# Optimization experiments

Measured on AMD Instinct MI355X. Metric: run time of the kernel, lower is better.

Reference implementation:

```python
import jax, jax.numpy as jnp
import numpy as np

SEQ, BATCH, D_MODEL, HEADS = 2048, 4, 1024, 16
D_K = D_MODEL // HEADS
SCALE = 1.0 / np.sqrt(D_K).astype(np.float32)


def setup_inputs() -> dict:
    key = jax.random.key(0)
    ks = jax.random.split(key, 12)
    s = 0.02
    inp = {
        "query": jax.random.normal(ks[0], (SEQ, BATCH, D_MODEL), jnp.float32),
        "key": jax.random.normal(ks[1], (SEQ, BATCH, D_MODEL), jnp.float32),
        "value": jax.random.normal(ks[2], (SEQ, BATCH, D_MODEL), jnp.float32),
        # causal mask [seq_q, seq_k, 1]; batch dim broadcasts per prepare_mask
        "mask": jnp.tril(jnp.ones((SEQ, SEQ), jnp.int32))[:, :, None],
        "Wq": jax.random.normal(ks[3], (D_MODEL, D_MODEL), jnp.float32) * s,
        "bq": jnp.zeros((D_MODEL,), jnp.float32),
        "Wk": jax.random.normal(ks[4], (D_MODEL, D_MODEL), jnp.float32) * s,
        "bk": jnp.zeros((D_MODEL,), jnp.float32),
        "Wv": jax.random.normal(ks[5], (D_MODEL, D_MODEL), jnp.float32) * s,
        "bv": jnp.zeros((D_MODEL,), jnp.float32),
        "Wo": jax.random.normal(ks[6], (D_MODEL, D_MODEL), jnp.float32) * s,
        "bo": jnp.zeros((D_MODEL,), jnp.float32),
    }
    return inp


def _heads(x, W, b):
    # [s, b, d_model] -> [s, b, h, d_k]
    y = jnp.einsum('sbd,de->sbe', x, W.T) + b
    return y.reshape(x.shape[0], x.shape[1], HEADS, D_K)


def reference(query, key, value, mask, Wq, bq, Wk, bk, Wv, bv, Wo, bo):
    seq_len, batch_size, _ = query.shape
    q = _heads(query, Wq, bq)
    k = _heads(key, Wk, bk)
    v = _heads(value, Wv, bv)
    # scores [i, j, b, h]
    scores = jnp.einsum('ibhd,jbhd->ijbh', q, k) * SCALE
    m = mask[:, :, :, None]  # [sq, sk, b_or_1, 1]
    scores = jnp.where(m == 0, jnp.float32(-jnp.inf), scores)
    attn = jax.nn.softmax(scores, axis=1)  # softmax over key dim j
    x = jnp.einsum('ijbh,jbhd->ibhd', attn, v)
    x = x.reshape(seq_len, batch_size, D_MODEL)
    return jnp.einsum('sbd,de->sbe', x, Wo.T) + bo
```

## Files before the change

### kernel.cpp

```cpp
#include <hip/hip_runtime.h>
#include <hip/hip_bf16.h>

#define SEQ 2048
#define BATCH 4
#define DM 1024
#define HEADS 16
#define DK 64
#define NBH 64
#define SC_LOG2E (0.125f * 1.4426950408889634f)

typedef unsigned short u16;
typedef __attribute__((ext_vector_type(8))) short bf16x8;
typedef __attribute__((ext_vector_type(4))) float f32x4;

__device__ inline u16 f2bf(float f) {
    unsigned int u = __builtin_bit_cast(unsigned int, f);
    u += 0x7fffu + ((u >> 16) & 1u);
    return (u16)(u >> 16);
}
__device__ inline float fexp2(float x) {
    float r; asm("v_exp_f32 %0, %1" : "=v"(r) : "v"(x)); return r;
}
__device__ inline unsigned pkbf(float a, float b) {
    unsigned r; asm("v_cvt_pk_bf16_f32 %0, %1, %2" : "=v"(r) : "v"(a), "v"(b)); return r;
}

__global__ __launch_bounds__(256)
void conv_bf16(const float* __restrict__ q, const float* __restrict__ k,
               const float* __restrict__ v, const float* __restrict__ wq,
               const float* __restrict__ wk, const float* __restrict__ wv,
               const float* __restrict__ wo,
               u16* __restrict__ oq, u16* __restrict__ ok, u16* __restrict__ ov,
               u16* __restrict__ ow)
{
    const size_t A8 = (size_t)SEQ * BATCH * DM / 8;
    const size_t W8 = (size_t)DM * DM / 8;
    const size_t total = 3 * A8 + 4 * W8;
    for (size_t i = (size_t)blockIdx.x * 256 + threadIdx.x; i < total;
         i += (size_t)gridDim.x * 256) {
        const float* src; u16* dst; size_t off;
        if (i < A8)          { src = q; dst = oq; off = i; }
        else if (i < 2 * A8) { src = k; dst = ok; off = i - A8; }
        else if (i < 3 * A8) { src = v; dst = ov; off = i - 2 * A8; }
        else {
            size_t j = i - 3 * A8;
            int wsel = (int)(j >> 17);
            off = j & (W8 - 1);
            src = wsel == 0 ? wq : wsel == 1 ? wk : wsel == 2 ? wv : wo;
            dst = ow + (size_t)wsel * DM * DM;
        }
        float4 a = ((const float4*)src)[off * 2];
        float4 b = ((const float4*)src)[off * 2 + 1];
        uint4 w;
        w.x = pkbf(a.x, a.y); w.y = pkbf(a.z, a.w);
        w.z = pkbf(b.x, b.y); w.w = pkbf(b.z, b.w);
        *(uint4*)(dst + off * 8) = w;
    }
}

__device__ inline void gstage(const u16* __restrict__ src, u16* dst,
                              int wave, int lane) {
    #pragma unroll
    for (int i = 0; i < 4; ++i) {
        int ci = (i * 4 + wave) * 64 + lane;
        int row = ci >> 3, ch = ci & 7;
        const u16* g = src + (size_t)row * 1024 + ((ch ^ (row & 7)) << 3);
        u16* l = dst + (i * 4 + wave) * 512;
        __builtin_amdgcn_global_load_lds(
            (const __attribute__((address_space(1))) unsigned int*)g,
            (__attribute__((address_space(3))) unsigned int*)l, 16, 0, 0);
    }
}
__device__ inline bf16x8 rdt(const u16* t, int row, int ch) {
    return *(const bf16x8*)(t + row * 64 + ((ch ^ (row & 7)) << 3));
}

template<int MODE>
__global__ __launch_bounds__(256, 2)
void gemm_bf(const u16* __restrict__ A, const u16* __restrict__ B,
             const float* __restrict__ bias, void* __restrict__ Out, float oscale)
{
    __shared__ __align__(16) u16 sA[2][128 * 64];
    __shared__ __align__(16) u16 sB[2][128 * 64];
    const int tid  = threadIdx.x;
    const int lane = tid & 63, wave = tid >> 6;
    const int wr = (wave >> 1) * 64, wc = (wave & 1) * 64;
    const int l15 = lane & 15, lg = lane >> 4;
    const int row0 = blockIdx.x * 128, col0 = blockIdx.y * 128;
    const u16* Abase = A + (size_t)row0 * 1024;
    const u16* Bbase = B + (size_t)col0 * 1024;

    f32x4 acc[4][4];
    #pragma unroll
    for (int m = 0; m < 4; ++m)
        #pragma unroll
        for (int n = 0; n < 4; ++n) acc[m][n] = (f32x4){0.f, 0.f, 0.f, 0.f};

    gstage(Abase, sA[0], wave, lane);
    gstage(Bbase, sB[0], wave, lane);
    __syncthreads();

    int cur = 0;
    for (int kt = 0; kt < 16; ++kt) {
        if (kt < 15) {
            gstage(Abase + (kt + 1) * 64, sA[cur ^ 1], wave, lane);
            gstage(Bbase + (kt + 1) * 64, sB[cur ^ 1], wave, lane);
        }
        #pragma unroll
        for (int s = 0; s < 2; ++s) {
            bf16x8 af[4], bf[4];
            #pragma unroll
            for (int m = 0; m < 4; ++m)
                af[m] = rdt(sA[cur], wr + m * 16 + l15, s * 4 + lg);
            #pragma unroll
            for (int n = 0; n < 4; ++n)
                bf[n] = rdt(sB[cur], wc + n * 16 + l15, s * 4 + lg);
            __builtin_amdgcn_s_setprio(1);
            #pragma unroll
            for (int m = 0; m < 4; ++m)
                #pragma unroll
                for (int n = 0; n < 4; ++n)
                    acc[m][n] = __builtin_amdgcn_mfma_f32_16x16x32_bf16(
                        af[m], bf[n], acc[m][n], 0, 0, 0);
            __builtin_amdgcn_s_setprio(0);
        }
        __syncthreads();
        cur ^= 1;
    }

    #pragma unroll
    for (int m = 0; m < 4; ++m) {
        #pragma unroll
        for (int n = 0; n < 4; ++n) {
            #pragma unroll
            for (int r = 0; r < 4; ++r) {
                int R = row0 + wr + m * 16 + lg * 4 + r;
                int E = col0 + wc + n * 16 + l15;
                float v = (acc[m][n][r] + bias[E]) * oscale;
                if (MODE == 2) {
                    ((float*)Out)[(size_t)R * 1024 + E] = v;
                } else {
                    int s = R >> 2, b = R & 3, hh = E >> 6, d = E & 63;
                    size_t idx = (MODE == 0)
                        ? ((size_t)(b * HEADS + hh) * SEQ + s) * DK + d
                        : ((size_t)(b * HEADS + hh) * DK + d) * SEQ + s;
                    ((u16*)Out)[idx] = f2bf(v);
                }
            }
        }
    }
}

__device__ inline void stage_tile(const u16* __restrict__ srcRow0, int srcStride,
                                  u16* tile, int wave, int lane) {
    #pragma unroll
    for (int i = 0; i < 2; ++i) {
        int row = wave * 16 + i * 8 + (lane >> 3);
        int chunk = (lane & 7) ^ (row & 7);
        const u16* g = srcRow0 + (size_t)row * srcStride + chunk * 8;
        u16* l = tile + (wave * 16 + i * 8) * 64;
        __builtin_amdgcn_global_load_lds(
            (const __attribute__((address_space(1))) unsigned int*)g,
            (__attribute__((address_space(3))) unsigned int*)l, 16, 0, 0);
    }
}
__device__ inline bf16x8 tread(const u16* tile, int row, int chunk) {
    return *(const bf16x8*)((const char*)tile + row * 128 + ((chunk ^ (row & 7)) << 4));
}

__global__ __launch_bounds__(256, 4)
void attn_fwd(const u16* __restrict__ Q, const u16* __restrict__ K,
              const u16* __restrict__ V, u16* __restrict__ X)
{
    __shared__ __align__(16) u16 sK[2][4096];
    __shared__ __align__(16) u16 sV[2][4096];
    __shared__ __align__(16) u16 plds[4][16 * 64];

    const int lin = blockIdx.x + 16 * blockIdx.y;
    const int xcd = lin & 7, ii = lin >> 3;
    const int bh  = (ii & 7) | (xcd << 3);
    const int tA  = ii >> 3;
    const int tB  = 31 - tA;
    const int b = bh >> 4, h = bh & 15;
    const int lane = threadIdx.x & 63, wave = threadIdx.x >> 6;
    const int l15 = lane & 15, lg = lane >> 4;
    const int qloc = wave * 16 + l15;
    const int swz  = (l15 & 7) << 4;
    const u16* Qh = Q + (size_t)bh * SEQ * DK;
    const u16* Kh = K + (size_t)bh * SEQ * DK;
    const u16* Vh = V + (size_t)bh * SEQ * DK;

    const int qA = tA * 64 + wave * 16, qB = tB * 64 + wave * 16;
    const bf16x8 qfA0 = *(const bf16x8*)&Qh[(size_t)(qA + l15) * DK + lg * 8];
    const bf16x8 qfA1 = *(const bf16x8*)&Qh[(size_t)(qA + l15) * DK + 32 + lg * 8];
    const bf16x8 qfB0 = *(const bf16x8*)&Qh[(size_t)(qB + l15) * DK + lg * 8];
    const bf16x8 qfB1 = *(const bf16x8*)&Qh[(size_t)(qB + l15) * DK + 32 + lg * 8];

    f32x4 oA[4], oB[4];
    #pragma unroll
    for (int n = 0; n < 4; ++n) {
        oA[n] = (f32x4){0.f, 0.f, 0.f, 0.f};
        oB[n] = (f32x4){0.f, 0.f, 0.f, 0.f};
    }
    float lsA = 0.f, lsB = 0.f;

    u16* pw = &plds[wave][0];

    auto compute = [&](const u16* kt, const u16* vt,
                       const bf16x8& q0v, const bf16x8& q1v,
                       f32x4* o, float& ls, bool diag) {
        f32x4 sc[4];
        #pragma unroll
        for (int c = 0; c < 4; ++c) sc[c] = (f32x4){0.f, 0.f, 0.f, 0.f};

        __builtin_amdgcn_s_setprio(1);
        #pragma unroll
        for (int c = 0; c < 4; ++c) {
            bf16x8 k0 = tread(kt, 16 * c + l15, lg);
            bf16x8 k1 = tread(kt, 16 * c + l15, 4 + lg);
            sc[c] = __builtin_amdgcn_mfma_f32_16x16x32_bf16(k0, q0v, sc[c], 0, 0, 0);
            sc[c] = __builtin_amdgcn_mfma_f32_16x16x32_bf16(k1, q1v, sc[c], 0, 0, 0);
        }
        __builtin_amdgcn_s_setprio(0);

        #pragma unroll
        for (int c = 0; c < 4; ++c) {
            float p[4];
            #pragma unroll
            for (int r = 0; r < 4; ++r) {
                float e = fexp2(sc[c][r]);
                if (diag) {
                    int kl = 16 * c + 4 * lg + r;
                    e = (kl <= qloc) ? e : 0.f;
                }
                p[r] = e;
                ls += e;
            }
            uint2 w;
            w.x = pkbf(p[0], p[1]);
            w.y = pkbf(p[2], p[3]);
            *(uint2*)((char*)pw + l15 * 128 + ((32 * c + 8 * lg) ^ swz)) = w;
        }
        asm volatile("s_waitcnt lgkmcnt(0)" ::: "memory");
        __builtin_amdgcn_sched_barrier(0);
        bf16x8 pf0 = *(const bf16x8*)((const char*)pw + l15 * 128 + ((16 * lg) ^ swz));
        bf16x8 pf1 = *(const bf16x8*)((const char*)pw + l15 * 128 + ((64 + 16 * lg) ^ swz));

        __builtin_amdgcn_s_setprio(1);
        #pragma unroll
        for (int n = 0; n < 4; ++n) {
            bf16x8 v0 = tread(vt, 16 * n + l15, lg);
            bf16x8 v1 = tread(vt, 16 * n + l15, 4 + lg);
            o[n] = __builtin_amdgcn_mfma_f32_16x16x32_bf16(pf0, v0, o[n], 0, 0, 0);
            o[n] = __builtin_amdgcn_mfma_f32_16x16x32_bf16(pf1, v1, o[n], 0, 0, 0);
        }
        __builtin_amdgcn_s_setprio(0);
    };

    stage_tile(Kh, DK, sK[0], wave, lane);
    stage_tile(Vh, SEQ, sV[0], wave, lane);
    __syncthreads();

    const int nst = tB + 1;
    int cur = 0;
    for (int blk = 0; blk < nst; ++blk) {
        if (blk + 1 < nst) {
            const int j1 = (blk + 1) * 64;
            stage_tile(Kh + (size_t)j1 * DK, DK, sK[cur ^ 1], wave, lane);
            stage_tile(Vh + j1, SEQ, sV[cur ^ 1], wave, lane);
        }
        if (blk <= tA)
            compute(sK[cur], sV[cur], qfA0, qfA1, oA, lsA, blk == tA);
        compute(sK[cur], sV[cur], qfB0, qfB1, oB, lsB, blk == tB);
        __syncthreads();
        cur ^= 1;
    }

    auto finish = [&](f32x4* o, float ls, int q0) {
        float tot = ls;
        tot += __shfl_xor(tot, 16, 64);
        tot += __shfl_xor(tot, 32, 64);
        float inv[4];
        #pragma unroll
        for (int r = 0; r < 4; ++r)
            inv[r] = 1.0f / __shfl(tot, lg * 4 + r, 64);
        #pragma unroll
        for (int n = 0; n < 4; ++n)
            #pragma unroll
            for (int r = 0; r < 4; ++r) {
                const int i = q0 + lg * 4 + r;
                X[((size_t)i * BATCH + b) * DM + h * DK + 16 * n + l15] =
                    f2bf(o[n][r] * inv[r]);
            }
    };
    finish(oA, lsA, qA);
    finish(oB, lsB, qB);
}

extern "C" void kernel_launch(void* const* d_in, const int* in_sizes, int n_in,
                              void* d_out, int out_size, void* d_ws, size_t ws_size,
                              hipStream_t stream) {
    const float* query = (const float*)d_in[0];
    const float* key   = (const float*)d_in[1];
    const float* value = (const float*)d_in[2];
    const float* Wq = (const float*)d_in[4];
    const float* bq = (const float*)d_in[5];
    const float* Wk = (const float*)d_in[6];
    const float* bk = (const float*)d_in[7];
    const float* Wv = (const float*)d_in[8];
    const float* bv = (const float*)d_in[9];
    const float* Wo = (const float*)d_in[10];
    const float* bo = (const float*)d_in[11];

    const size_t NELEM = (size_t)SEQ * BATCH * DM;
    const size_t WM    = (size_t)DM * DM;
    u16* S0  = (u16*)d_ws;
    u16* S1  = S0 + NELEM;
    u16* S2  = S1 + NELEM;
    u16* S3  = S2 + NELEM;
    u16* Wbf = S3 + NELEM;

    dim3 gg(64, 8), gb(256);
    hipLaunchKernelGGL(conv_bf16, dim3(2048), gb, 0, stream,
                       query, key, value, Wq, Wk, Wv, Wo, S0, S1, S2, Wbf);
    hipLaunchKernelGGL((gemm_bf<0>), gg, gb, 0, stream, S0, Wbf,          bq, S3, SC_LOG2E);
    hipLaunchKernelGGL((gemm_bf<0>), gg, gb, 0, stream, S1, Wbf + WM,     bk, S0, 1.0f);
    hipLaunchKernelGGL((gemm_bf<1>), gg, gb, 0, stream, S2, Wbf + 2 * WM, bv, S1, 1.0f);
    hipLaunchKernelGGL(attn_fwd, dim3(16, NBH), gb, 0, stream, S3, S0, S1, S2);
    hipLaunchKernelGGL((gemm_bf<2>), gg, gb, 0, stream, S2, Wbf + 3 * WM, bo, (float*)d_out, 1.0f);
}
```

Before: 176.7 us.

## Pair adjacent query tiles per block and interleave their MFMAs on shared K/V

Each block now takes two adjacent 64-row query tiles (t16*128 and +64) instead of the mirrored pair tA and 31-tA. One loop over key tiles runs QK^T and PV for both query tiles on each staged K/V tile, so both reuse the same LDS reads and their independent MFMAs can interleave. The explicit lgkmcnt wait and sched barrier before reading P are dropped, giving the scheduler more freedom. In exchange, work per block is no longer balanced (2 to 32 iterations); blocks are launched heaviest first to soften the tail.

Measured after the change: 184.1 us. 1.04x slower.

```diff
diff --git a/kernel.cpp b/kernel.cpp
--- a/kernel.cpp
+++ b/kernel.cpp
@@ -177,20 +177,20 @@
     __shared__ __align__(16) u16 plds[4][16 * 64];
 
     const int lin = blockIdx.x + 16 * blockIdx.y;
-    const int xcd = lin & 7, ii = lin >> 3;
-    const int bh  = (ii & 7) | (xcd << 3);
-    const int tA  = ii >> 3;
-    const int tB  = 31 - tA;
+    const int xcd = lin & 7;
+    const int bh  = xcd * 8 + ((lin >> 3) & 7);
+    const int t16 = 15 - (lin >> 6);
     const int b = bh >> 4, h = bh & 15;
     const int lane = threadIdx.x & 63, wave = threadIdx.x >> 6;
     const int l15 = lane & 15, lg = lane >> 4;
     const int qloc = wave * 16 + l15;
-    const int swz  = (l15 & 7) << 4;
+    const int swz = (l15 & 7) << 4;
     const u16* Qh = Q + (size_t)bh * SEQ * DK;
     const u16* Kh = K + (size_t)bh * SEQ * DK;
     const u16* Vh = V + (size_t)bh * SEQ * DK;
 
-    const int qA = tA * 64 + wave * 16, qB = tB * 64 + wave * 16;
+    const int qA = t16 * 128 + wave * 16;
+    const int qB = qA + 64;
     const bf16x8 qfA0 = *(const bf16x8*)&Qh[(size_t)(qA + l15) * DK + lg * 8];
     const bf16x8 qfA1 = *(const bf16x8*)&Qh[(size_t)(qA + l15) * DK + 32 + lg * 8];
     const bf16x8 qfB0 = *(const bf16x8*)&Qh[(size_t)(qB + l15) * DK + lg * 8];
@@ -203,26 +203,9 @@
         oB[n] = (f32x4){0.f, 0.f, 0.f, 0.f};
     }
     float lsA = 0.f, lsB = 0.f;
-
     u16* pw = &plds[wave][0];
 
-    auto compute = [&](const u16* kt, const u16* vt,
-                       const bf16x8& q0v, const bf16x8& q1v,
-                       f32x4* o, float& ls, bool diag) {
-        f32x4 sc[4];
-        #pragma unroll
-        for (int c = 0; c < 4; ++c) sc[c] = (f32x4){0.f, 0.f, 0.f, 0.f};
-
-        __builtin_amdgcn_s_setprio(1);
-        #pragma unroll
-        for (int c = 0; c < 4; ++c) {
-            bf16x8 k0 = tread(kt, 16 * c + l15, lg);
-            bf16x8 k1 = tread(kt, 16 * c + l15, 4 + lg);
-            sc[c] = __builtin_amdgcn_mfma_f32_16x16x32_bf16(k0, q0v, sc[c], 0, 0, 0);
-            sc[c] = __builtin_amdgcn_mfma_f32_16x16x32_bf16(k1, q1v, sc[c], 0, 0, 0);
-        }
-        __builtin_amdgcn_s_setprio(0);
-
+    auto expack = [&](f32x4* sc, bool diag, float& ls, bf16x8& pf0, bf16x8& pf1) {
         #pragma unroll
         for (int c = 0; c < 4; ++c) {
             float p[4];
@@ -241,37 +224,63 @@
             w.y = pkbf(p[2], p[3]);
             *(uint2*)((char*)pw + l15 * 128 + ((32 * c + 8 * lg) ^ swz)) = w;
         }
-        asm volatile("s_waitcnt lgkmcnt(0)" ::: "memory");
-        __builtin_amdgcn_sched_barrier(0);
-        bf16x8 pf0 = *(const bf16x8*)((const char*)pw + l15 * 128 + ((16 * lg) ^ swz));
-        bf16x8 pf1 = *(const bf16x8*)((const char*)pw + l15 * 128 + ((64 + 16 * lg) ^ swz));
+        pf0 = *(const bf16x8*)((const char*)pw + l15 * 128 + ((16 * lg) ^ swz));
+        pf1 = *(const bf16x8*)((const char*)pw + l15 * 128 + ((64 + 16 * lg) ^ swz));
+    };
+
+    const int NB = 2 * t16 + 2;
+    stage_tile(Kh, DK, sK[0], wave, lane);
+    stage_tile(Vh, SEQ, sV[0], wave, lane);
+    __syncthreads();
+
+    int cur = 0;
+    for (int j = 0; j < NB; ++j) {
+        if (j + 1 < NB) {
+            stage_tile(Kh + (size_t)(j + 1) * 64 * DK, DK, sK[cur ^ 1], wave, lane);
+            stage_tile(Vh + (j + 1) * 64, SEQ, sV[cur ^ 1], wave, lane);
+        }
+        const u16* kt = sK[cur];
+        const u16* vt = sV[cur];
+        const bool hasA = (j < NB - 1);
+
+        f32x4 scA[4], scB[4];
+        #pragma unroll
+        for (int c = 0; c < 4; ++c) {
+            scA[c] = (f32x4){0.f, 0.f, 0.f, 0.f};
+            scB[c] = (f32x4){0.f, 0.f, 0.f, 0.f};
+        }
+        __builtin_amdgcn_s_setprio(1);
+        #pragma unroll
+        for (int c = 0; c < 4; ++c) {
+            bf16x8 k0 = tread(kt, 16 * c + l15, lg);
+            bf16x8 k1 = tread(kt, 16 * c + l15, 4 + lg);
+            scB[c] = __builtin_amdgcn_mfma_f32_16x16x32_bf16(k0, qfB0, scB[c], 0, 0, 0);
+            scB[c] = __builtin_amdgcn_mfma_f32_16x16x32_bf16(k1, qfB1, scB[c], 0, 0, 0);
+            if (hasA) {
+                scA[c] = __builtin_amdgcn_mfma_f32_16x16x32_bf16(k0, qfA0, scA[c], 0, 0, 0);
+                scA[c] = __builtin_amdgcn_mfma_f32_16x16x32_bf16(k1, qfA1, scA[c], 0, 0, 0);
+            }
+        }
+        __builtin_amdgcn_s_setprio(0);
+
+        bf16x8 pfA0, pfA1, pfB0, pfB1;
+        expack(scB, j == NB - 1, lsB, pfB0, pfB1);
+        if (hasA) expack(scA, j == NB - 2, lsA, pfA0, pfA1);
 
         __builtin_amdgcn_s_setprio(1);
         #pragma unroll
         for (int n = 0; n < 4; ++n) {
             bf16x8 v0 = tread(vt, 16 * n + l15, lg);
             bf16x8 v1 = tread(vt, 16 * n + l15, 4 + lg);
-            o[n] = __builtin_amdgcn_mfma_f32_16x16x32_bf16(pf0, v0, o[n], 0, 0, 0);
-            o[n] = __builtin_amdgcn_mfma_f32_16x16x32_bf16(pf1, v1, o[n], 0, 0, 0);
+            oB[n] = __builtin_amdgcn_mfma_f32_16x16x32_bf16(pfB0, v0, oB[n], 0, 0, 0);
+            oB[n] = __builtin_amdgcn_mfma_f32_16x16x32_bf16(pfB1, v1, oB[n], 0, 0, 0);
+            if (hasA) {
+                oA[n] = __builtin_amdgcn_mfma_f32_16x16x32_bf16(pfA0, v0, oA[n], 0, 0, 0);
+                oA[n] = __builtin_amdgcn_mfma_f32_16x16x32_bf16(pfA1, v1, oA[n], 0, 0, 0);
+            }
         }
         __builtin_amdgcn_s_setprio(0);
-    };
-
-    stage_tile(Kh, DK, sK[0], wave, lane);
-    stage_tile(Vh, SEQ, sV[0], wave, lane);
-    __syncthreads();
-
-    const int nst = tB + 1;
-    int cur = 0;
-    for (int blk = 0; blk < nst; ++blk) {
-        if (blk + 1 < nst) {
-            const int j1 = (blk + 1) * 64;
-            stage_tile(Kh + (size_t)j1 * DK, DK, sK[cur ^ 1], wave, lane);
-            stage_tile(Vh + j1, SEQ, sV[cur ^ 1], wave, lane);
-        }
-        if (blk <= tA)
-            compute(sK[cur], sV[cur], qfA0, qfA1, oA, lsA, blk == tA);
-        compute(sK[cur], sV[cur], qfB0, qfB1, oB, lsB, blk == tB);
+
         __syncthreads();
         cur ^= 1;
     }
```

## Halve GEMM K-tile to 32 with new swizzle and raise occupancy to 4

Applied to the files above, without the earlier changes.

The projection GEMM now stages K-slices of 32 instead of 64, which halves its shared memory per block (32KB instead of 64KB). It uses a new swizzled LDS layout that packs two rows per 64-element line, and launch bounds go from 2 to 4 blocks per CU so more blocks can hide latency. The cost is twice as many K iterations and barriers with less MFMA work between them, plus tighter register limits that could cause spills with the 64-register accumulator tile. The attention kernel changes are cosmetic only.

Result: slower. 192.3 us (+8.8%).

```diff
diff --git a/kernel.cpp b/kernel.cpp
--- a/kernel.cpp
+++ b/kernel.cpp
@@ -58,30 +58,34 @@
     }
 }
 
-__device__ inline void gstage(const u16* __restrict__ src, u16* dst,
-                              int wave, int lane) {
-    #pragma unroll
-    for (int i = 0; i < 4; ++i) {
+__device__ inline void gstage32(const u16* __restrict__ src, u16* dst,
+                                int wave, int lane) {
+    #pragma unroll
+    for (int i = 0; i < 2; ++i) {
         int ci = (i * 4 + wave) * 64 + lane;
-        int row = ci >> 3, ch = ci & 7;
-        const u16* g = src + (size_t)row * 1024 + ((ch ^ (row & 7)) << 3);
+        int rho = ci >> 3, cpos = ci & 7;
+        int c0 = cpos ^ (rho & 7);
+        int arow = 2 * rho + (c0 >> 2), kc = c0 & 3;
+        const u16* g = src + (size_t)arow * 1024 + kc * 8;
         u16* l = dst + (i * 4 + wave) * 512;
         __builtin_amdgcn_global_load_lds(
             (const __attribute__((address_space(1))) unsigned int*)g,
             (__attribute__((address_space(3))) unsigned int*)l, 16, 0, 0);
     }
 }
-__device__ inline bf16x8 rdt(const u16* t, int row, int ch) {
-    return *(const bf16x8*)(t + row * 64 + ((ch ^ (row & 7)) << 3));
+__device__ inline bf16x8 rdt32(const u16* t, int row, int lg) {
+    int rho = row >> 1;
+    int cp = (((row & 1) << 2) | lg) ^ (rho & 7);
+    return *(const bf16x8*)(t + rho * 64 + cp * 8);
 }
 
 template<int MODE>
-__global__ __launch_bounds__(256, 2)
+__global__ __launch_bounds__(256, 4)
 void gemm_bf(const u16* __restrict__ A, const u16* __restrict__ B,
              const float* __restrict__ bias, void* __restrict__ Out, float oscale)
 {
-    __shared__ __align__(16) u16 sA[2][128 * 64];
-    __shared__ __align__(16) u16 sB[2][128 * 64];
+    __shared__ __align__(16) u16 sA[2][4096];
+    __shared__ __align__(16) u16 sB[2][4096];
     const int tid  = threadIdx.x;
     const int lane = tid & 63, wave = tid >> 6;
     const int wr = (wave >> 1) * 64, wc = (wave & 1) * 64;
@@ -96,34 +100,31 @@
         #pragma unroll
         for (int n = 0; n < 4; ++n) acc[m][n] = (f32x4){0.f, 0.f, 0.f, 0.f};
 
-    gstage(Abase, sA[0], wave, lane);
-    gstage(Bbase, sB[0], wave, lane);
+    gstage32(Abase, sA[0], wave, lane);
+    gstage32(Bbase, sB[0], wave, lane);
     __syncthreads();
 
     int cur = 0;
-    for (int kt = 0; kt < 16; ++kt) {
-        if (kt < 15) {
-            gstage(Abase + (kt + 1) * 64, sA[cur ^ 1], wave, lane);
-            gstage(Bbase + (kt + 1) * 64, sB[cur ^ 1], wave, lane);
-        }
-        #pragma unroll
-        for (int s = 0; s < 2; ++s) {
-            bf16x8 af[4], bf[4];
-            #pragma unroll
-            for (int m = 0; m < 4; ++m)
-                af[m] = rdt(sA[cur], wr + m * 16 + l15, s * 4 + lg);
+    for (int kt = 0; kt < 32; ++kt) {
+        if (kt < 31) {
+            gstage32(Abase + (kt + 1) * 32, sA[cur ^ 1], wave, lane);
+            gstage32(Bbase + (kt + 1) * 32, sB[cur ^ 1], wave, lane);
+        }
+        bf16x8 af[4], bf[4];
+        #pragma unroll
+        for (int m = 0; m < 4; ++m)
+            af[m] = rdt32(sA[cur], wr + m * 16 + l15, lg);
+        #pragma unroll
+        for (int n = 0; n < 4; ++n)
+            bf[n] = rdt32(sB[cur], wc + n * 16 + l15, lg);
+        __builtin_amdgcn_s_setprio(1);
+        #pragma unroll
+        for (int m = 0; m < 4; ++m)
             #pragma unroll
             for (int n = 0; n < 4; ++n)
-                bf[n] = rdt(sB[cur], wc + n * 16 + l15, s * 4 + lg);
-            __builtin_amdgcn_s_setprio(1);
-            #pragma unroll
-            for (int m = 0; m < 4; ++m)
-                #pragma unroll
-                for (int n = 0; n < 4; ++n)
-                    acc[m][n] = __builtin_amdgcn_mfma_f32_16x16x32_bf16(
-                        af[m], bf[n], acc[m][n], 0, 0, 0);
-            __builtin_amdgcn_s_setprio(0);
-        }
+                acc[m][n] = __builtin_amdgcn_mfma_f32_16x16x32_bf16(
+                    af[m], bf[n], acc[m][n], 0, 0, 0);
+        __builtin_amdgcn_s_setprio(0);
         __syncthreads();
         cur ^= 1;
     }
@@ -185,7 +186,7 @@
     const int lane = threadIdx.x & 63, wave = threadIdx.x >> 6;
     const int l15 = lane & 15, lg = lane >> 4;
     const int qloc = wave * 16 + l15;
-    const int swz  = (l15 & 7) << 4;
+    const int swz = (l15 & 7) << 4;
     const u16* Qh = Q + (size_t)bh * SEQ * DK;
     const u16* Kh = K + (size_t)bh * SEQ * DK;
     const u16* Vh = V + (size_t)bh * SEQ * DK;
@@ -203,7 +204,6 @@
         oB[n] = (f32x4){0.f, 0.f, 0.f, 0.f};
     }
     float lsA = 0.f, lsB = 0.f;
-
     u16* pw = &plds[wave][0];
 
     auto compute = [&](const u16* kt, const u16* vt,
@@ -265,9 +265,8 @@
     int cur = 0;
     for (int blk = 0; blk < nst; ++blk) {
         if (blk + 1 < nst) {
-            const int j1 = (blk + 1) * 64;
-            stage_tile(Kh + (size_t)j1 * DK, DK, sK[cur ^ 1], wave, lane);
-            stage_tile(Vh + j1, SEQ, sV[cur ^ 1], wave, lane);
+            stage_tile(Kh + (size_t)(blk + 1) * 64 * DK, DK, sK[cur ^ 1], wave, lane);
+            stage_tile(Vh + (blk + 1) * 64, SEQ, sV[cur ^ 1], wave, lane);
         }
         if (blk <= tA)
             compute(sK[cur], sV[cur], qfA0, qfA1, oA, lsA, blk == tA);
```

## Fuse fp32-to-bf16 activation conversion into projection GEMM A-tile loading

Applied to the files above, without the earlier changes.

Activations are no longer converted to bf16 in a separate pass. The Q/K/V projection GEMMs now read fp32 rows directly into registers, pack them to bf16 and write them swizzled into LDS, with the write interleaved between the two k-halves of the MFMA loop. The conversion kernel now handles only the four weight matrices. This removes a full read and write of three 32 MB activation tensors, at the cost of twice the global bytes per A tile inside the GEMM and extra VGPR pressure from holding eight float4 prefetches.

Measured after the change: 238.7 us. +35.1%, slower.

```diff
diff --git a/kernel.cpp b/kernel.cpp
--- a/kernel.cpp
+++ b/kernel.cpp
@@ -26,36 +26,22 @@
 }
 
 __global__ __launch_bounds__(256)
-void conv_bf16(const float* __restrict__ q, const float* __restrict__ k,
-               const float* __restrict__ v, const float* __restrict__ wq,
-               const float* __restrict__ wk, const float* __restrict__ wv,
-               const float* __restrict__ wo,
-               u16* __restrict__ oq, u16* __restrict__ ok, u16* __restrict__ ov,
-               u16* __restrict__ ow)
+void conv_w(const float* __restrict__ wq, const float* __restrict__ wk,
+            const float* __restrict__ wv, const float* __restrict__ wo,
+            u16* __restrict__ ow)
 {
-    const size_t A8 = (size_t)SEQ * BATCH * DM / 8;
     const size_t W8 = (size_t)DM * DM / 8;
-    const size_t total = 3 * A8 + 4 * W8;
-    for (size_t i = (size_t)blockIdx.x * 256 + threadIdx.x; i < total;
-         i += (size_t)gridDim.x * 256) {
-        const float* src; u16* dst; size_t off;
-        if (i < A8)          { src = q; dst = oq; off = i; }
-        else if (i < 2 * A8) { src = k; dst = ok; off = i - A8; }
-        else if (i < 3 * A8) { src = v; dst = ov; off = i - 2 * A8; }
-        else {
-            size_t j = i - 3 * A8;
-            int wsel = (int)(j >> 17);
-            off = j & (W8 - 1);
-            src = wsel == 0 ? wq : wsel == 1 ? wk : wsel == 2 ? wv : wo;
-            dst = ow + (size_t)wsel * DM * DM;
-        }
-        float4 a = ((const float4*)src)[off * 2];
-        float4 b = ((const float4*)src)[off * 2 + 1];
-        uint4 w;
-        w.x = pkbf(a.x, a.y); w.y = pkbf(a.z, a.w);
-        w.z = pkbf(b.x, b.y); w.w = pkbf(b.z, b.w);
-        *(uint4*)(dst + off * 8) = w;
-    }
+    size_t i = (size_t)blockIdx.x * 256 + threadIdx.x;
+    int wsel = (int)(i >> 17);
+    size_t off = i & (W8 - 1);
+    const float* src = wsel == 0 ? wq : wsel == 1 ? wk : wsel == 2 ? wv : wo;
+    u16* dst = ow + (size_t)wsel * DM * DM;
+    float4 a = ((const float4*)src)[off * 2];
+    float4 b = ((const float4*)src)[off * 2 + 1];
+    uint4 w;
+    w.x = pkbf(a.x, a.y); w.y = pkbf(a.z, a.w);
+    w.z = pkbf(b.x, b.y); w.w = pkbf(b.z, b.w);
+    *(uint4*)(dst + off * 8) = w;
 }
 
 __device__ inline void gstage(const u16* __restrict__ src, u16* dst,
@@ -73,6 +59,32 @@
 }
 __device__ inline bf16x8 rdt(const u16* t, int row, int ch) {
     return *(const bf16x8*)(t + row * 64 + ((ch ^ (row & 7)) << 3));
+}
+
+template<int MODE>
+__device__ inline void gemm_epilogue(f32x4 acc[4][4], const float* bias,
+                                     void* Out, float oscale,
+                                     int row0, int col0, int wr, int wc,
+                                     int lg, int l15) {
+    #pragma unroll
+    for (int m = 0; m < 4; ++m)
+        #pragma unroll
+        for (int n = 0; n < 4; ++n)
+            #pragma unroll
+            for (int r = 0; r < 4; ++r) {
+                int R = row0 + wr + m * 16 + lg * 4 + r;
+                int E = col0 + wc + n * 16 + l15;
+                float v = (acc[m][n][r] + bias[E]) * oscale;
+                if (MODE == 2) {
+                    ((float*)Out)[(size_t)R * 1024 + E] = v;
+                } else {
+                    int s = R >> 2, b = R & 3, hh = E >> 6, d = E & 63;
+                    size_t idx = (MODE == 0)
+                        ? ((size_t)(b * HEADS + hh) * SEQ + s) * DK + d
+                        : ((size_t)(b * HEADS + hh) * DK + d) * SEQ + s;
+                    ((u16*)Out)[idx] = f2bf(v);
+                }
+            }
 }
 
 template<int MODE>
@@ -127,28 +139,104 @@
         __syncthreads();
         cur ^= 1;
     }
-
-    #pragma unroll
-    for (int m = 0; m < 4; ++m) {
-        #pragma unroll
-        for (int n = 0; n < 4; ++n) {
-            #pragma unroll
-            for (int r = 0; r < 4; ++r) {
-                int R = row0 + wr + m * 16 + lg * 4 + r;
-                int E = col0 + wc + n * 16 + l15;
-                float v = (acc[m][n][r] + bias[E]) * oscale;
-                if (MODE == 2) {
-                    ((float*)Out)[(size_t)R * 1024 + E] = v;
-                } else {
-                    int s = R >> 2, b = R & 3, hh = E >> 6, d = E & 63;
-                    size_t idx = (MODE == 0)
-                        ? ((size_t)(b * HEADS + hh) * SEQ + s) * DK + d
-                        : ((size_t)(b * HEADS + hh) * DK + d) * SEQ + s;
-                    ((u16*)Out)[idx] = f2bf(v);
-                }
-            }
-        }
-    }
+    gemm_epilogue<MODE>(acc, bias, Out, oscale, row0, col0, wr, wc, lg, l15);
+}
+
+template<int MODE>
+__global__ __launch_bounds__(256, 2)
+void gemm_af32(const float* __restrict__ A, const u16* __restrict__ B,
+               const float* __restrict__ bias, void* __restrict__ Out, float oscale)
+{
+    __shared__ __align__(16) u16 sA[2][128 * 64];
+    __shared__ __align__(16) u16 sB[2][128 * 64];
+    const int tid  = threadIdx.x;
+    const int lane = tid & 63, wave = tid >> 6;
+    const int wr = (wave >> 1) * 64, wc = (wave & 1) * 64;
+    const int l15 = lane & 15, lg = lane >> 4;
+    const int row0 = blockIdx.x * 128, col0 = blockIdx.y * 128;
+    const int arow = tid >> 1, ahalf = tid & 1;
+    const float* Ag = A + (size_t)(row0 + arow) * 1024 + ahalf * 32;
+    const u16* Bbase = B + (size_t)col0 * 1024;
+
+    f32x4 acc[4][4];
+    #pragma unroll
+    for (int m = 0; m < 4; ++m)
+        #pragma unroll
+        for (int n = 0; n < 4; ++n) acc[m][n] = (f32x4){0.f, 0.f, 0.f, 0.f};
+
+    auto loadA = [&](int kt, float4* r) {
+        const float4* p = (const float4*)(Ag + kt * 64);
+        #pragma unroll
+        for (int j = 0; j < 8; ++j) r[j] = p[j];
+    };
+    auto writeA = [&](const float4* r, u16* dst) {
+        #pragma unroll
+        for (int j = 0; j < 4; ++j) {
+            uint4 w;
+            w.x = pkbf(r[2 * j].x, r[2 * j].y);
+            w.y = pkbf(r[2 * j].z, r[2 * j].w);
+            w.z = pkbf(r[2 * j + 1].x, r[2 * j + 1].y);
+            w.w = pkbf(r[2 * j + 1].z, r[2 * j + 1].w);
+            int cp = (4 * ahalf + j) ^ (arow & 7);
+            *(uint4*)(dst + arow * 64 + cp * 8) = w;
+        }
+    };
+
+    {
+        float4 a0[8];
+        loadA(0, a0);
+        gstage(Bbase, sB[0], wave, lane);
+        writeA(a0, sA[0]);
+    }
+    __syncthreads();
+
+    int cur = 0;
+    for (int kt = 0; kt < 16; ++kt) {
+        float4 an[8];
+        const bool pre = (kt < 15);
+        if (pre) {
+            loadA(kt + 1, an);
+            gstage(Bbase + (kt + 1) * 64, sB[cur ^ 1], wave, lane);
+        }
+        {
+            bf16x8 af[4], bf[4];
+            #pragma unroll
+            for (int m = 0; m < 4; ++m)
+                af[m] = rdt(sA[cur], wr + m * 16 + l15, lg);
+            #pragma unroll
+            for (int n = 0; n < 4; ++n)
+                bf[n] = rdt(sB[cur], wc + n * 16 + l15, lg);
+            __builtin_amdgcn_s_setprio(1);
+            #pragma unroll
+            for (int m = 0; m < 4; ++m)
+                #pragma unroll
+                for (int n = 0; n < 4; ++n)
+                    acc[m][n] = __builtin_amdgcn_mfma_f32_16x16x32_bf16(
+                        af[m], bf[n], acc[m][n], 0, 0, 0);
+            __builtin_amdgcn_s_setprio(0);
+        }
+        if (pre) writeA(an, sA[cur ^ 1]);
+        {
+            bf16x8 af[4], bf[4];
+            #pragma unroll
+            for (int m = 0; m < 4; ++m)
+                af[m] = rdt(sA[cur], wr + m * 16 + l15, 4 + lg);
+            #pragma unroll
+            for (int n = 0; n < 4; ++n)
+                bf[n] = rdt(sB[cur], wc + n * 16 + l15, 4 + lg);
+            __builtin_amdgcn_s_setprio(1);
+            #pragma unroll
+            for (int m = 0; m < 4; ++m)
+                #pragma unroll
+                for (int n = 0; n < 4; ++n)
+                    acc[m][n] = __builtin_amdgcn_mfma_f32_16x16x32_bf16(
+                        af[m], bf[n], acc[m][n], 0, 0, 0);
+            __builtin_amdgcn_s_setprio(0);
+        }
+        __syncthreads();
+        cur ^= 1;
+    }
+    gemm_epilogue<MODE>(acc, bias, Out, oscale, row0, col0, wr, wc, lg, l15);
 }
 
 __device__ inline void stage_tile(const u16* __restrict__ srcRow0, int srcStride,
@@ -185,7 +273,7 @@
     const int lane = threadIdx.x & 63, wave = threadIdx.x >> 6;
     const int l15 = lane & 15, lg = lane >> 4;
     const int qloc = wave * 16 + l15;
-    const int swz  = (l15 & 7) << 4;
+    const int swz = (l15 & 7) << 4;
     const u16* Qh = Q + (size_t)bh * SEQ * DK;
     const u16* Kh = K + (size_t)bh * SEQ * DK;
     const u16* Vh = V + (size_t)bh * SEQ * DK;
@@ -203,7 +291,6 @@
         oB[n] = (f32x4){0.f, 0.f, 0.f, 0.f};
     }
     float lsA = 0.f, lsB = 0.f;
-
     u16* pw = &plds[wave][0];
 
     auto compute = [&](const u16* kt, const u16* vt,
@@ -265,9 +352,8 @@
     int cur = 0;
     for (int blk = 0; blk < nst; ++blk) {
         if (blk + 1 < nst) {
-            const int j1 = (blk + 1) * 64;
-            stage_tile(Kh + (size_t)j1 * DK, DK, sK[cur ^ 1], wave, lane);
-            stage_tile(Vh + j1, SEQ, sV[cur ^ 1], wave, lane);
+            stage_tile(Kh + (size_t)(blk + 1) * 64 * DK, DK, sK[cur ^ 1], wave, lane);
+            stage_tile(Vh + (blk + 1) * 64, SEQ, sV[cur ^ 1], wave, lane);
         }
         if (blk <= tA)
             compute(sK[cur], sV[cur], qfA0, qfA1, oA, lsA, blk == tA);
@@ -314,18 +400,17 @@
 
     const size_t NELEM = (size_t)SEQ * BATCH * DM;
     const size_t WM    = (size_t)DM * DM;
-    u16* S0  = (u16*)d_ws;
-    u16* S1  = S0 + NELEM;
-    u16* S2  = S1 + NELEM;
-    u16* S3  = S2 + NELEM;
-    u16* Wbf = S3 + NELEM;
+    u16* Qb  = (u16*)d_ws;
+    u16* Kb  = Qb + NELEM;
+    u16* Vt  = Kb + NELEM;
+    u16* Xb  = Vt + NELEM;
+    u16* Wbf = Xb + NELEM;
 
     dim3 gg(64, 8), gb(256);
-    hipLaunchKernelGGL(conv_bf16, dim3(2048), gb, 0, stream,
-                       query, key, value, Wq, Wk, Wv, Wo, S0, S1, S2, Wbf);
-    hipLaunchKernelGGL((gemm_bf<0>), gg, gb, 0, stream, S0, Wbf,          bq, S3, SC_LOG2E);
-    hipLaunchKernelGGL((gemm_bf<0>), gg, gb, 0, stream, S1, Wbf + WM,     bk, S0, 1.0f);
-    hipLaunchKernelGGL((gemm_bf<1>), gg, gb, 0, stream, S2, Wbf + 2 * WM, bv, S1, 1.0f);
-    hipLaunchKernelGGL(attn_fwd, dim3(16, NBH), gb, 0, stream, S3, S0, S1, S2);
-    hipLaunchKernelGGL((gemm_bf<2>), gg, gb, 0, stream, S2, Wbf + 3 * WM, bo, (float*)d_out, 1.0f);
-}
+    hipLaunchKernelGGL(conv_w, dim3(2048), gb, 0, stream, Wq, Wk, Wv, Wo, Wbf);
+    hipLaunchKernelGGL((gemm_af32<0>), gg, gb, 0, stream, query, Wbf,          bq, Qb, SC_LOG2E);
+    hipLaunchKernelGGL((gemm_af32<0>), gg, gb, 0, stream, key,   Wbf + WM,     bk, Kb, 1.0f);
+    hipLaunchKernelGGL((gemm_af32<1>), gg, gb, 0, stream, value, Wbf + 2 * WM, bv, Vt, 1.0f);
+    hipLaunchKernelGGL(attn_fwd, dim3(16, NBH), gb, 0, stream, Qb, Kb, Vt, Xb);
+    hipLaunchKernelGGL((gemm_bf<2>),   gg, gb, 0, stream, Xb, Wbf + 3 * WM, bo, (float*)d_out, 1.0f);
+}
```
